# Kernel tuning notes

Measured on AMD Instinct MI355X. Metric: run time of the kernel, lower is better.

## Reference

```python
import jax, jax.numpy as jnp
import numpy as np

NUM_EXPERTS = 8
TOP_K = 2

def setup_inputs() -> dict:
    key = jax.random.key(0)
    ks = jax.random.split(key, 5)
    B, S, D, F, E = 4, 2048, 1024, 4096, NUM_EXPERTS
    x = jax.random.normal(ks[0], (B, S, D), dtype=jnp.float32)
    router_w = jax.random.normal(ks[1], (D, E), dtype=jnp.float32) * 0.02
    router_b = jnp.zeros((E,), dtype=jnp.float32)
    w1 = jax.random.normal(ks[2], (E, D, F), dtype=jnp.float32) * 0.02
    b1 = jnp.zeros((E, F), dtype=jnp.float32)
    w2 = jax.random.normal(ks[3], (E, F, D), dtype=jnp.float32) * 0.02
    b2 = jnp.zeros((E, D), dtype=jnp.float32)
    return {"x": x, "router_w": router_w, "router_b": router_b,
            "w1": w1, "b1": b1, "w2": w2, "b2": b2}

def reference(x, router_w, router_b, w1, b1, w2, b2):
    B, S, D = x.shape
    E = router_w.shape[1]
    x_flat = x.reshape(-1, D)                                  # [N, D]
    router_probs = jax.nn.softmax(x_flat @ router_w + router_b, axis=-1)  # [N, E]
    topk_probs, topk_idx = jax.lax.top_k(router_probs, TOP_K)  # [N, K]
    topk_probs = topk_probs / jnp.sum(topk_probs, axis=-1, keepdims=True)
    # combine weight per (token, expert): sum over top-k slots assigned to that expert
    cw = jnp.sum(topk_probs[..., None] * jax.nn.one_hot(topk_idx, E, dtype=x.dtype), axis=1)  # [N, E]
    out = jnp.zeros_like(x_flat)
    for e in range(E):  # small fixed expert count; each iter is a dense GEMM pair
        h = jax.nn.gelu(x_flat @ w1[e] + b1[e], approximate=False)  # [N, F]
        out = out + cw[:, e:e + 1] * (h @ w2[e] + b2[e])            # [N, D]
    return out.reshape(B, S, D)
```

## Files before the change

### kernel.cpp

```cpp
#include <hip/hip_runtime.h>
#include <hip/hip_bf16.h>

typedef __attribute__((ext_vector_type(8))) __bf16 bf16x8;
typedef __attribute__((ext_vector_type(4))) float f32x4;

#define NTOK 8192
#define D_DIM 1024
#define F_DIM 4096
#define NEXP 8
#define SLOT_TOT 16384
#define SLOT_CAP 16640
#define TILE_MAX 136

__device__ __forceinline__ unsigned short f2b(float f) {
  __hip_bfloat16 b = __float2bfloat16(f);
  return reinterpret_cast<unsigned short&>(b);
}

__device__ __forceinline__ float gelu_f(float v) {
  const float y2 = v * (1.5957691216f + 0.0713548162f * v * v);
  return v * __builtin_amdgcn_rcpf(1.f + __expf(-y2));
}

__device__ __forceinline__ void gload_lds16(const void* g, void* l) {
  __builtin_amdgcn_global_load_lds(
      (__attribute__((address_space(1))) void*)g,
      (__attribute__((address_space(3))) void*)l, 16, 0, 0);
}


__global__ void init_counts_kernel(int* counts) {
  if (threadIdx.x < NEXP) counts[threadIdx.x] = 0;
}

__global__ void zero_out_kernel(float* out) {
  const int i = blockIdx.x * 256 + threadIdx.x;
  reinterpret_cast<float4*>(out)[i] = make_float4(0.f, 0.f, 0.f, 0.f);
}

__global__ void gather_x_kernel(const float* __restrict__ x,
                                const int* __restrict__ slot_token,
                                __hip_bfloat16* __restrict__ xg) {
  const int s = blockIdx.x;
  const int t = slot_token[s];
  const int d = threadIdx.x * 4;
  const float4 v = *reinterpret_cast<const float4*>(x + (size_t)t * D_DIM + d);
  union { unsigned short u[4]; uint2 q; } o;
  o.u[0] = f2b(v.x); o.u[1] = f2b(v.y); o.u[2] = f2b(v.z); o.u[3] = f2b(v.w);
  *reinterpret_cast<uint2*>(xg + (size_t)s * D_DIM + d) = o.q;
}

__global__ void combine_kernel(const __hip_bfloat16* __restrict__ ys,
                               const int* __restrict__ slot_pos,
                               const float* __restrict__ topk_w,
                               float* __restrict__ out) {
  const int tok = blockIdx.x;
  const int d = threadIdx.x * 4;
  const int s0 = slot_pos[tok * 2], s1 = slot_pos[tok * 2 + 1];
  const float w0 = topk_w[tok * 2], w1 = topk_w[tok * 2 + 1];
  union { unsigned short u[4]; uint2 q; } a, b;
  a.q = *reinterpret_cast<const uint2*>(ys + (size_t)s0 * D_DIM + d);
  b.q = *reinterpret_cast<const uint2*>(ys + (size_t)s1 * D_DIM + d);
  float4 rr;
  float va[4];
  #pragma unroll
  for (int i = 0; i < 4; ++i) {
    unsigned int ua = (unsigned int)a.u[i] << 16;
    unsigned int ub = (unsigned int)b.u[i] << 16;
    va[i] = w0 * reinterpret_cast<float&>(ua) + w1 * reinterpret_cast<float&>(ub);
  }
  rr.x = va[0]; rr.y = va[1]; rr.z = va[2]; rr.w = va[3];
  *reinterpret_cast<float4*>(out + (size_t)tok * D_DIM + d) = rr;
}

__global__ void transpose_conv_kernel(const float* __restrict__ src,
                                      __hip_bfloat16* __restrict__ dst,
                                      int R, int C) {
  __shared__ float tile[64][65];
  const int e = blockIdx.z;
  src += (size_t)e * R * C;
  dst += (size_t)e * R * C;
  const int c0 = blockIdx.x * 64, r0 = blockIdx.y * 64;
  const int tx = threadIdx.x, ty = threadIdx.y;
  #pragma unroll
  for (int j = 0; j < 4; ++j) {
    const float4 v = *reinterpret_cast<const float4*>(
        &src[(size_t)(r0 + ty + j * 16) * C + c0 + tx * 4]);
    tile[ty + j * 16][tx * 4 + 0] = v.x;
    tile[ty + j * 16][tx * 4 + 1] = v.y;
    tile[ty + j * 16][tx * 4 + 2] = v.z;
    tile[ty + j * 16][tx * 4 + 3] = v.w;
  }
  __syncthreads();
  #pragma unroll
  for (int j = 0; j < 4; ++j) {
    const int c = ty + j * 16;
    union { unsigned short u[4]; uint2 d; } o;
    #pragma unroll
    for (int i = 0; i < 4; ++i) o.u[i] = f2b(tile[tx * 4 + i][c]);
    *reinterpret_cast<uint2*>(&dst[(size_t)(c0 + c) * R + r0 + tx * 4]) = o.d;
  }
}

__global__ void router_kernel(const float* __restrict__ x,
                              const float* __restrict__ rw,
                              const float* __restrict__ rb,
                              int* __restrict__ topk_idx,
                              float* __restrict__ topk_w,
                              int* __restrict__ counts) {
  __shared__ float rwT[NEXP * D_DIM];
  const int tid = threadIdx.x;
  for (int i = tid; i < NEXP * D_DIM; i += 256) {
    const int d = i >> 3, e = i & 7;
    rwT[e * D_DIM + d] = rw[i];
  }
  __syncthreads();

  const int wave = tid >> 6, lane = tid & 63;
  const int tok = blockIdx.x * 4 + wave;
  const float* xr = x + (size_t)tok * D_DIM;

  float acc[NEXP];
  #pragma unroll
  for (int e = 0; e < NEXP; ++e) acc[e] = 0.f;

  for (int i = 0; i < D_DIM / 64; ++i) {
    const int d = i * 64 + lane;
    const float xv = xr[d];
    #pragma unroll
    for (int e = 0; e < NEXP; ++e) acc[e] += xv * rwT[e * D_DIM + d];
  }
  #pragma unroll
  for (int off = 32; off > 0; off >>= 1) {
    #pragma unroll
    for (int e = 0; e < NEXP; ++e) acc[e] += __shfl_xor(acc[e], off);
  }

  if (lane == 0) {
    float l[NEXP];
    #pragma unroll
    for (int e = 0; e < NEXP; ++e) l[e] = acc[e] + rb[e];
    int i1 = 0;
    #pragma unroll
    for (int e = 1; e < NEXP; ++e) if (l[e] > l[i1]) i1 = e;
    int i2 = (i1 == 0) ? 1 : 0;
    #pragma unroll
    for (int e = 0; e < NEXP; ++e) if (e != i1 && e != i2 && l[e] > l[i2]) i2 = e;
    const float w1 = 1.f / (1.f + __expf(l[i2] - l[i1]));
    topk_idx[tok * 2 + 0] = i1;
    topk_idx[tok * 2 + 1] = i2;
    topk_w[tok * 2 + 0] = w1;
    topk_w[tok * 2 + 1] = 1.f - w1;
    atomicAdd(&counts[i1], 1);
    atomicAdd(&counts[i2], 1);
  }
}

__global__ void offsets_kernel(const int* __restrict__ counts,
                               int* __restrict__ offsets,
                               int* __restrict__ cursors,
                               int* __restrict__ slot_token,
                               int* __restrict__ tile_meta) {
  const int t = threadIdx.x;
  if (t == 0) {
    int s = 0;
    for (int e = 0; e < NEXP; ++e) { offsets[e] = s; cursors[e] = s; s += counts[e]; }
    offsets[NEXP] = s;
    int n = 0;
    for (int e = 0; e < NEXP; ++e) {
      const int nt = (counts[e] + 127) >> 7;
      for (int m = 0; m < nt && n < TILE_MAX; ++m) tile_meta[n++] = e | (m << 8);
    }
    for (; n < TILE_MAX; ++n) tile_meta[n] = 0 | (1 << 22);
  }
  if (t < SLOT_CAP - SLOT_TOT) {
    slot_token[SLOT_TOT + t] = 0;
  }
}

__global__ void scatter_kernel(const int* __restrict__ topk_idx,
                               int* __restrict__ cursors,
                               int* __restrict__ slot_token,
                               int* __restrict__ slot_pos) {
  const int tok = blockIdx.x * 256 + threadIdx.x;
  if (tok >= NTOK) return;
  #pragma unroll
  for (int k = 0; k < 2; ++k) {
    const int e = topk_idx[tok * 2 + k];
    const int p = atomicAdd(&cursors[e], 1);
    slot_token[p] = tok;
    slot_pos[tok * 2 + k] = p;
  }
}

template <int PHASE>
__global__ __launch_bounds__(256, 5) void moe_gemm(
    const __hip_bfloat16* __restrict__ A,
    const __hip_bfloat16* __restrict__ B,
    const float* __restrict__ bias,
    const int* __restrict__ counts,
    const int* __restrict__ offsets,
    const int* __restrict__ tile_meta,
    __hip_bfloat16* __restrict__ Cout) {
  constexpr int K    = (PHASE == 1) ? D_DIM : F_DIM;
  constexpr int NCOL = (PHASE == 1) ? F_DIM : D_DIM;
  constexpr int NT   = NCOL / 128;
  constexpr int KT   = K / 32;

  const int bid = blockIdx.x;
  const int j = bid / NT, nt = bid % NT;
  const int meta = tile_meta[j];
  const int e = meta & 255, mt = meta >> 8;
  const int cnt = counts[e];
  if (mt * 128 >= cnt) return;
  const int base = offsets[e];

  __shared__ unsigned short lds[2][8192];

  const int tid = threadIdx.x;
  const int w = tid >> 6, lane = tid & 63;
  const int r = lane & 15, kg = lane >> 4;
  const int wm = w >> 1, wn = w & 1;

  const __hip_bfloat16* gA0 = A + (size_t)(base + mt * 128 + w * 16 + r) * K + kg * 8;
  const __hip_bfloat16* gA1 = gA0 + (size_t)64 * K;
  const __hip_bfloat16* gB0 = B + ((size_t)e * NCOL + nt * 128 + w * 16 + r) * K + kg * 8;
  const __hip_bfloat16* gB1 = gB0 + (size_t)64 * K;

  f32x4 acc[4][4] = {};

  auto stage = [&](unsigned short* buf) {
    gload_lds16(gA0, buf + w * 512);
    gload_lds16(gA1, buf + (w + 4) * 512);
    gload_lds16(gB0, buf + 4096 + w * 512);
    gload_lds16(gB1, buf + 4096 + (w + 4) * 512);
    gA0 += 32; gA1 += 32; gB0 += 32; gB1 += 32;
  };
  auto compute = [&](const unsigned short* buf) {
    bf16x8 af[4], bfr[4];
    #pragma unroll
    for (int i2 = 0; i2 < 4; ++i2) {
      af[i2]  = *(const bf16x8*)(buf + (wm * 4 + i2) * 512 + lane * 8);
      bfr[i2] = *(const bf16x8*)(buf + 4096 + (wn * 4 + i2) * 512 + lane * 8);
    }
    #pragma unroll
    for (int mi = 0; mi < 4; ++mi)
      #pragma unroll
      for (int ni = 0; ni < 4; ++ni)
        acc[mi][ni] = __builtin_amdgcn_mfma_f32_16x16x32_bf16(
            af[mi], bfr[ni], acc[mi][ni], 0, 0, 0);
  };

  unsigned short* pc = lds[0];
  unsigned short* pn = lds[1];

  stage(pc);
  for (int t = 0; t < KT - 1; ++t) {
    stage(pn);
    __builtin_amdgcn_sched_barrier(0);
    asm volatile("s_waitcnt vmcnt(4)" ::: "memory");
    __builtin_amdgcn_sched_barrier(0);
    __builtin_amdgcn_s_barrier();
    compute(pc);
    __builtin_amdgcn_sched_barrier(0);
    __builtin_amdgcn_s_barrier();
    unsigned short* ts = pc; pc = pn; pn = ts;
  }
  asm volatile("s_waitcnt vmcnt(0)" ::: "memory");
  __builtin_amdgcn_sched_barrier(0);
  __builtin_amdgcn_s_barrier();
  compute(pc);

  const int rem = cnt - mt * 128;
  const int q4 = (lane >> 4) * 4;
  const int c15 = lane & 15;

  if (rem >= 128) {
    #pragma unroll
    for (int n = 0; n < 4; ++n) {
      const int col = nt * 128 + wn * 64 + n * 16 + c15;
      const float bv = bias[e * NCOL + col];
      #pragma unroll
      for (int m = 0; m < 4; ++m) {
        #pragma unroll
        for (int rr = 0; rr < 4; ++rr) {
          const int rloc = wm * 64 + m * 16 + q4 + rr;
          float v = acc[m][n][rr] + bv;
          if constexpr (PHASE == 1) v = gelu_f(v);
          Cout[(size_t)(base + mt * 128 + rloc) * NCOL + col] = __float2bfloat16(v);
        }
      }
    }
  } else {
    #pragma unroll
    for (int n = 0; n < 4; ++n) {
      const int col = nt * 128 + wn * 64 + n * 16 + c15;
      const float bv = bias[e * NCOL + col];
      #pragma unroll
      for (int m = 0; m < 4; ++m) {
        #pragma unroll
        for (int rr = 0; rr < 4; ++rr) {
          const int rloc = wm * 64 + m * 16 + q4 + rr;
          if (rloc < rem) {
            float v = acc[m][n][rr] + bv;
            if constexpr (PHASE == 1) v = gelu_f(v);
            Cout[(size_t)(base + mt * 128 + rloc) * NCOL + col] = __float2bfloat16(v);
          }
        }
      }
    }
  }
}


extern "C" void kernel_launch(void* const* d_in, const int* in_sizes, int n_in,
                              void* d_out, int out_size, void* d_ws, size_t ws_size,
                              hipStream_t stream) {
  const float* x  = (const float*)d_in[0];
  const float* rw = (const float*)d_in[1];
  const float* rb = (const float*)d_in[2];
  const float* w1 = (const float*)d_in[3];
  const float* b1 = (const float*)d_in[4];
  const float* w2 = (const float*)d_in[5];
  const float* b2 = (const float*)d_in[6];
  float* out = (float*)d_out;

  char* p = (char*)d_ws;
  size_t used = 0;
  auto carve = [&](size_t bytes) {
    char* r = p + used;
    used += (bytes + 255) & ~(size_t)255;
    return (void*)r;
  };
  __hip_bfloat16* xg  = (__hip_bfloat16*)carve((size_t)SLOT_CAP * D_DIM * 2);
  __hip_bfloat16* ys  = xg;
  __hip_bfloat16* w1t = (__hip_bfloat16*)carve((size_t)NEXP * F_DIM * D_DIM * 2);
  __hip_bfloat16* w2t = (__hip_bfloat16*)carve((size_t)NEXP * D_DIM * F_DIM * 2);
  __hip_bfloat16* h   = (__hip_bfloat16*)carve((size_t)SLOT_CAP * F_DIM * 2);
  int*   topk_idx   = (int*)carve((size_t)NTOK * 2 * 4);
  float* topk_w     = (float*)carve((size_t)NTOK * 2 * 4);
  int*   slot_token = (int*)carve((size_t)SLOT_CAP * 4);
  int*   slot_pos   = (int*)carve((size_t)NTOK * 2 * 4);
  int*   tile_meta  = (int*)carve(TILE_MAX * 4);
  int* counts  = (int*)carve(256);
  int* offsets = (int*)carve(256);
  int* cursors = (int*)carve(256);

  if (used > ws_size) {
    zero_out_kernel<<<8192, 256, 0, stream>>>(out);
    return;
  }

  init_counts_kernel<<<1, 64, 0, stream>>>(counts);
  router_kernel<<<NTOK / 4, 256, 0, stream>>>(x, rw, rb, topk_idx, topk_w, counts);
  offsets_kernel<<<1, 256, 0, stream>>>(counts, offsets, cursors, slot_token, tile_meta);
  scatter_kernel<<<NTOK / 256, 256, 0, stream>>>(topk_idx, cursors, slot_token, slot_pos);
  gather_x_kernel<<<SLOT_CAP, 256, 0, stream>>>(x, slot_token, xg);

  dim3 tb(16, 16);
  transpose_conv_kernel<<<dim3(F_DIM / 64, D_DIM / 64, NEXP), tb, 0, stream>>>(w1, w1t, D_DIM, F_DIM);
  transpose_conv_kernel<<<dim3(D_DIM / 64, F_DIM / 64, NEXP), tb, 0, stream>>>(w2, w2t, F_DIM, D_DIM);

  moe_gemm<1><<<TILE_MAX * (F_DIM / 128), 256, 0, stream>>>(
      xg, w1t, b1, counts, offsets, tile_meta, h);
  moe_gemm<2><<<TILE_MAX * (D_DIM / 128), 256, 0, stream>>>(
      h, w2t, b2, counts, offsets, tile_meta, ys);

  combine_kernel<<<NTOK, 256, 0, stream>>>(ys, slot_pos, topk_w, out);
}
```

Baseline: 987.8 us.

## Triple-buffer GEMM LDS pipeline and replace tile_meta with static expert-interleaved grid

The MoE grouped GEMM moves from a double-buffered to a triple-buffered LDS pipeline, keeping two K-tiles of loads in flight, and raises MFMA issue priority around the compute block. The data-dependent tile_meta table is removed. Blocks are now mapped statically, with the expert in the low bits and a fixed MT_MAX of 64 row tiles per expert, and blocks past an expert's count exit early. This interleaves experts across the grid and drops the serial metadata build, at the cost of launching many empty blocks. Occupancy drops to 3 blocks per CU because of the larger LDS footprint.

New measurement: 995.0 us. About the same (+0.7%).

```diff
diff --git a/kernel.cpp b/kernel.cpp
--- a/kernel.cpp
+++ b/kernel.cpp
@@ -10,7 +10,10 @@
 #define NEXP 8
 #define SLOT_TOT 16384
 #define SLOT_CAP 16640
-#define TILE_MAX 136
+#define MT_MAX 32
+
+#undef MT_MAX
+#define MT_MAX 64
 
 __device__ __forceinline__ unsigned short f2b(float f) {
   __hip_bfloat16 b = __float2bfloat16(f);
@@ -159,19 +162,12 @@
 __global__ void offsets_kernel(const int* __restrict__ counts,
                                int* __restrict__ offsets,
                                int* __restrict__ cursors,
-                               int* __restrict__ slot_token,
-                               int* __restrict__ tile_meta) {
+                               int* __restrict__ slot_token) {
   const int t = threadIdx.x;
   if (t == 0) {
     int s = 0;
     for (int e = 0; e < NEXP; ++e) { offsets[e] = s; cursors[e] = s; s += counts[e]; }
     offsets[NEXP] = s;
-    int n = 0;
-    for (int e = 0; e < NEXP; ++e) {
-      const int nt = (counts[e] + 127) >> 7;
-      for (int m = 0; m < nt && n < TILE_MAX; ++m) tile_meta[n++] = e | (m << 8);
-    }
-    for (; n < TILE_MAX; ++n) tile_meta[n] = 0 | (1 << 22);
   }
   if (t < SLOT_CAP - SLOT_TOT) {
     slot_token[SLOT_TOT + t] = 0;
@@ -194,13 +190,12 @@
 }
 
 template <int PHASE>
-__global__ __launch_bounds__(256, 5) void moe_gemm(
+__global__ __launch_bounds__(256, 3) void moe_gemm(
     const __hip_bfloat16* __restrict__ A,
     const __hip_bfloat16* __restrict__ B,
     const float* __restrict__ bias,
     const int* __restrict__ counts,
     const int* __restrict__ offsets,
-    const int* __restrict__ tile_meta,
     __hip_bfloat16* __restrict__ Cout) {
   constexpr int K    = (PHASE == 1) ? D_DIM : F_DIM;
   constexpr int NCOL = (PHASE == 1) ? F_DIM : D_DIM;
@@ -208,14 +203,16 @@
   constexpr int KT   = K / 32;
 
   const int bid = blockIdx.x;
-  const int j = bid / NT, nt = bid % NT;
-  const int meta = tile_meta[j];
-  const int e = meta & 255, mt = meta >> 8;
+  const int e = bid & 7;
+  const int slot = bid >> 3;
+  int mt, nt;
+  if constexpr (PHASE == 1) { mt = slot & (MT_MAX - 1); nt = slot >> 6; }
+  else                      { nt = slot & (NT - 1);     mt = slot >> 3; }
   const int cnt = counts[e];
   if (mt * 128 >= cnt) return;
   const int base = offsets[e];
 
-  __shared__ unsigned short lds[2][8192];
+  __shared__ unsigned short lds[3][8192];
 
   const int tid = threadIdx.x;
   const int w = tid >> 6, lane = tid & 63;
@@ -243,33 +240,41 @@
       af[i2]  = *(const bf16x8*)(buf + (wm * 4 + i2) * 512 + lane * 8);
       bfr[i2] = *(const bf16x8*)(buf + 4096 + (wn * 4 + i2) * 512 + lane * 8);
     }
+    __builtin_amdgcn_s_setprio(1);
     #pragma unroll
     for (int mi = 0; mi < 4; ++mi)
       #pragma unroll
       for (int ni = 0; ni < 4; ++ni)
         acc[mi][ni] = __builtin_amdgcn_mfma_f32_16x16x32_bf16(
             af[mi], bfr[ni], acc[mi][ni], 0, 0, 0);
+    __builtin_amdgcn_s_setprio(0);
   };
 
-  unsigned short* pc = lds[0];
-  unsigned short* pn = lds[1];
-
-  stage(pc);
-  for (int t = 0; t < KT - 1; ++t) {
-    stage(pn);
+  unsigned short *p0 = lds[0], *p1 = lds[1], *p2 = lds[2];
+
+  stage(p0);
+  stage(p1);
+  for (int t = 0; t < KT - 2; ++t) {
+    stage(p2);
     __builtin_amdgcn_sched_barrier(0);
-    asm volatile("s_waitcnt vmcnt(4)" ::: "memory");
+    asm volatile("s_waitcnt vmcnt(8)" ::: "memory");
     __builtin_amdgcn_sched_barrier(0);
     __builtin_amdgcn_s_barrier();
-    compute(pc);
+    compute(p0);
     __builtin_amdgcn_sched_barrier(0);
     __builtin_amdgcn_s_barrier();
-    unsigned short* ts = pc; pc = pn; pn = ts;
-  }
+    unsigned short* ts = p0; p0 = p1; p1 = p2; p2 = ts;
+  }
+  asm volatile("s_waitcnt vmcnt(4)" ::: "memory");
+  __builtin_amdgcn_sched_barrier(0);
+  __builtin_amdgcn_s_barrier();
+  compute(p0);
+  __builtin_amdgcn_sched_barrier(0);
+  __builtin_amdgcn_s_barrier();
   asm volatile("s_waitcnt vmcnt(0)" ::: "memory");
   __builtin_amdgcn_sched_barrier(0);
   __builtin_amdgcn_s_barrier();
-  compute(pc);
+  compute(p1);
 
   const int rem = cnt - mt * 128;
   const int q4 = (lane >> 4) * 4;
@@ -341,7 +346,6 @@
   float* topk_w     = (float*)carve((size_t)NTOK * 2 * 4);
   int*   slot_token = (int*)carve((size_t)SLOT_CAP * 4);
   int*   slot_pos   = (int*)carve((size_t)NTOK * 2 * 4);
-  int*   tile_meta  = (int*)carve(TILE_MAX * 4);
   int* counts  = (int*)carve(256);
   int* offsets = (int*)carve(256);
   int* cursors = (int*)carve(256);
@@ -353,7 +357,7 @@
 
   init_counts_kernel<<<1, 64, 0, stream>>>(counts);
   router_kernel<<<NTOK / 4, 256, 0, stream>>>(x, rw, rb, topk_idx, topk_w, counts);
-  offsets_kernel<<<1, 256, 0, stream>>>(counts, offsets, cursors, slot_token, tile_meta);
+  offsets_kernel<<<1, 256, 0, stream>>>(counts, offsets, cursors, slot_token);
   scatter_kernel<<<NTOK / 256, 256, 0, stream>>>(topk_idx, cursors, slot_token, slot_pos);
   gather_x_kernel<<<SLOT_CAP, 256, 0, stream>>>(x, slot_token, xg);
 
@@ -361,10 +365,10 @@
   transpose_conv_kernel<<<dim3(F_DIM / 64, D_DIM / 64, NEXP), tb, 0, stream>>>(w1, w1t, D_DIM, F_DIM);
   transpose_conv_kernel<<<dim3(D_DIM / 64, F_DIM / 64, NEXP), tb, 0, stream>>>(w2, w2t, F_DIM, D_DIM);
 
-  moe_gemm<1><<<TILE_MAX * (F_DIM / 128), 256, 0, stream>>>(
-      xg, w1t, b1, counts, offsets, tile_meta, h);
-  moe_gemm<2><<<TILE_MAX * (D_DIM / 128), 256, 0, stream>>>(
-      h, w2t, b2, counts, offsets, tile_meta, ys);
+  moe_gemm<1><<<NEXP * MT_MAX * (F_DIM / 128), 256, 0, stream>>>(
+      xg, w1t, b1, counts, offsets, h);
+  moe_gemm<2><<<NEXP * MT_MAX * (D_DIM / 128), 256, 0, stream>>>(
+      h, w2t, b2, counts, offsets, ys);
 
   combine_kernel<<<NTOK, 256, 0, stream>>>(ys, slot_pos, topk_w, out);
 }
```
